# Kernel tuning notes

Measured on AMD Instinct MI355X. Metric: run time of the kernel, lower is better.

Reference implementation:

```python
import jax, jax.numpy as jnp
import numpy as np

PAD = 1
THRESH = 10.0


def setup_inputs() -> dict:
    key = jax.random.key(0)
    k1, k2, k3 = jax.random.split(key, 3)
    x = jax.random.normal(k1, (8, 16, 62, 62), dtype=jnp.float32)
    W = jax.random.normal(k2, (32, 16, 3, 3), dtype=jnp.float32)
    b = jax.random.normal(k3, (32,), dtype=jnp.float32)
    return {"x": x, "W": W, "b": b}


def reference(x, W, b):
    # ZeroPad2d(padding) on all four sides
    x = jnp.pad(x, ((0, 0), (0, 0), (PAD, PAD), (PAD, PAD)))
    T, C, xr, xc = x.shape
    O, _, wr, wc = W.shape
    L = xr * xc

    # get_xfft_thresh: 1D FFT over flattened HxW, zero coeffs with |Re| < thresh
    xf = jnp.fft.fft(x.reshape(T, C, L))                      # (T,C,L) complex
    xf = jnp.where(jnp.abs(xf.real) < THRESH, jnp.zeros_like(xf), xf)

    # get_Wfft: zero-pad kernel to (xr,xc) bottom/right, flatten, reverse along
    # length (flipud(flip([0,1])) nets to a flip of the last axis only), then FFT
    Wp = jnp.pad(W, ((0, 0), (0, 0), (0, xr - wr), (0, xc - wc))).reshape(O, C, L)
    Wf = jnp.fft.fft(Wp[:, :, ::-1])                          # (O,C,L) complex

    # fftConv1D, batched over (image, out_channel):
    y = jnp.fft.ifft(xf[:, None, :, :] * Wf[None, :, :, :]).real  # (T,O,C,L)
    # torch.roll(y, 1) with no dims rolls the FLATTENED (C*L) tensor by 1
    y = jnp.roll(y.reshape(T, O, C * L), 1, axis=-1).reshape(T, O, C, xr, xc)
    y = y.sum(axis=2)                                         # sum over in-channels
    ans_r, ans_c = xr - wr + 1, xc - wc + 1
    y = y[:, :, :ans_r, :ans_c]
    return y + b[None, :, None, None]
```

## Files before the change

kernel.cpp:

```cpp
#include <hip/hip_runtime.h>
#include <math.h>

#define TWO_PI 6.28318530717958647692f
#define NT     512
#define WPB    8
#define RPW    8
#define PITCH  65
#define THRESH 10.0f

__device__ __forceinline__ int brev6(int x) {
    return (int)(__brev((unsigned)x) >> 26);
}

__device__ __forceinline__ void cfma(float& dr, float& di, float ar, float ai,
                                     float br, float bi) {
    dr = fmaf(ar, br, fmaf(-ai, bi, dr));
    di = fmaf(ar, bi, fmaf(ai, br, di));
}

__device__ __forceinline__ void fft64_dif(float (&re)[RPW], float (&im)[RPW],
                                          int lane, float sign) {
    #pragma unroll
    for (int h = 32; h >= 1; h >>= 1) {
        int j = lane & (h - 1);
        float ang = sign * (TWO_PI / 64.0f) * (float)(j * (32 / h));
        float wr, wi;
        __sincosf(ang, &wi, &wr);
        bool upper = (lane & h) != 0;
        float cwr = upper ? wr : 1.0f;
        float cwi = upper ? wi : 0.0f;
        float sgn = upper ? -1.0f : 1.0f;
        #pragma unroll
        for (int m = 0; m < RPW; ++m) {
            float orr = __shfl_xor(re[m], h, 64);
            float oii = __shfl_xor(im[m], h, 64);
            float ar = fmaf(sgn, re[m], orr);
            float ai = fmaf(sgn, im[m], oii);
            re[m] = ar * cwr - ai * cwi;
            im[m] = ar * cwi + ai * cwr;
        }
    }
}

__device__ __forceinline__ void fft64_dit(float (&re)[RPW], float (&im)[RPW],
                                          int lane, float sign) {
    #pragma unroll
    for (int h = 1; h <= 32; h <<= 1) {
        int j = lane & (h - 1);
        float ang = sign * (TWO_PI / 64.0f) * (float)(j * (32 / h));
        float wr, wi;
        __sincosf(ang, &wi, &wr);
        bool upper = (lane & h) != 0;
        float cwr = upper ? wr : 1.0f;
        float cwi = upper ? wi : 0.0f;
        float sgn = upper ? -1.0f : 1.0f;
        #pragma unroll
        for (int m = 0; m < RPW; ++m) {
            float tr = re[m] * cwr - im[m] * cwi;
            float ti = re[m] * cwi + im[m] * cwr;
            float orr = __shfl_xor(tr, h, 64);
            float oii = __shfl_xor(ti, h, 64);
            re[m] = fmaf(sgn, tr, orr);
            im[m] = fmaf(sgn, ti, oii);
        }
    }
}

__global__ __launch_bounds__(NT) void fwd_kernel(const float* __restrict__ x,
                                                 float2* __restrict__ X) {
    __shared__ float sre[64 * PITCH];
    __shared__ float sim[64 * PITCH];
    const int tc   = blockIdx.x;
    const int tid  = threadIdx.x;
    const int lane = tid & 63;
    const int w    = tid >> 6;
    const float* xrow = x + (size_t)tc * 62 * 62;

    for (int idx = tid; idx < 4096; idx += NT) {
        int r = idx >> 6, s = idx & 63;
        float v = 0.0f;
        if (r >= 1 && r <= 62 && s >= 1 && s <= 62)
            v = xrow[(r - 1) * 62 + (s - 1)];
        sre[r * PITCH + s] = v;
    }
    __syncthreads();

    float re[RPW], im[RPW];
    #pragma unroll
    for (int m = 0; m < RPW; ++m) {
        re[m] = sre[lane * PITCH + (w * RPW + m)];
        im[m] = 0.0f;
    }
    fft64_dif(re, im, lane, -1.0f);
    const int k1 = brev6(lane);
    #pragma unroll
    for (int m = 0; m < RPW; ++m) {
        int n2 = w * RPW + m;
        float cr, ci;
        __sincosf(-(TWO_PI / 4096.0f) * (float)(k1 * n2), &ci, &cr);
        float rr = re[m] * cr - im[m] * ci;
        im[m]    = re[m] * ci + im[m] * cr;
        re[m]    = rr;
    }
    __syncthreads();
    #pragma unroll
    for (int m = 0; m < RPW; ++m) {
        int n2 = w * RPW + m;
        sre[k1 * PITCH + n2] = re[m];
        sim[k1 * PITCH + n2] = im[m];
    }
    __syncthreads();
    #pragma unroll
    for (int m = 0; m < RPW; ++m) {
        int row = w * RPW + m;
        re[m] = sre[row * PITCH + lane];
        im[m] = sim[row * PITCH + lane];
    }
    fft64_dif(re, im, lane, -1.0f);
    float2* Xrow = X + (size_t)tc * 4096;
    #pragma unroll
    for (int m = 0; m < RPW; ++m) {
        int row = w * RPW + m;
        float rr = re[m], ii = im[m];
        if (fabsf(rr) < THRESH) { rr = 0.0f; ii = 0.0f; }
        Xrow[row * 64 + lane] = make_float2(rr, ii);
    }
}

__global__ __launch_bounds__(NT) void conv_kernel(const float2* __restrict__ X,
                                                  const float* __restrict__ W,
                                                  const float* __restrict__ b,
                                                  float* __restrict__ out) {
    __shared__ float sre[64 * PITCH];
    __shared__ float sim[64 * PITCH];
    __shared__ float Wsh[144];
    const int t    = blockIdx.x >> 5;
    const int o    = blockIdx.x & 31;
    const int tid  = threadIdx.x;
    const int lane = tid & 63;
    const int w    = tid >> 6;
    if (tid < 144) Wsh[tid] = W[o * 144 + tid];
    __syncthreads();

    const int k2 = brev6(lane);
    float elr, eli;
    __sincosf((TWO_PI / 64.0f) * (float)k2, &eli, &elr);

    float re[RPW], im[RPW];
    const float2* Xt = X + (size_t)t * 16 * 4096;
    #pragma unroll
    for (int m = 0; m < RPW; ++m) {
        const int k1 = w * RPW + m;
        float ur, ui, vkr, vki;
        __sincosf((TWO_PI / 64.0f) * (float)k1, &ui, &ur);
        __sincosf((TWO_PI / 4096.0f) * (float)k1, &vki, &vkr);
        float vr = vkr * elr - vki * eli;
        float vi = vkr * eli + vki * elr;
        float qr[9] = {0,0,0,0,0,0,0,0,0};
        float qi[9] = {0,0,0,0,0,0,0,0,0};
        const int p = k1 * 64 + lane;
        #pragma unroll
        for (int c = 0; c < 16; ++c) {
            float2 xc = Xt[c * 4096 + p];
            const float* wc = &Wsh[c * 9];
            #pragma unroll
            for (int q = 0; q < 9; ++q) {
                qr[q] = fmaf(wc[q], xc.x, qr[q]);
                qi[q] = fmaf(wc[q], xc.y, qi[q]);
            }
        }
        float R0r, R0i, R1r, R1i, R2r, R2i, tr_, ti_;
        tr_ = qr[2]; ti_ = qi[2];
        R0r = qr[1]; R0i = qi[1]; cfma(R0r, R0i, vr, vi, tr_, ti_);
        tr_ = R0r; ti_ = R0i;
        R0r = qr[0]; R0i = qi[0]; cfma(R0r, R0i, vr, vi, tr_, ti_);
        tr_ = qr[5]; ti_ = qi[5];
        R1r = qr[4]; R1i = qi[4]; cfma(R1r, R1i, vr, vi, tr_, ti_);
        tr_ = R1r; ti_ = R1i;
        R1r = qr[3]; R1i = qi[3]; cfma(R1r, R1i, vr, vi, tr_, ti_);
        tr_ = qr[8]; ti_ = qi[8];
        R2r = qr[7]; R2i = qi[7]; cfma(R2r, R2i, vr, vi, tr_, ti_);
        tr_ = R2r; ti_ = R2i;
        R2r = qr[6]; R2i = qi[6]; cfma(R2r, R2i, vr, vi, tr_, ti_);
        cfma(R1r, R1i, ur, ui, R2r, R2i);
        cfma(R0r, R0i, ur, ui, R1r, R1i);
        re[m] = R0r;
        im[m] = R0i;
    }
    fft64_dit(re, im, lane, +1.0f);
    #pragma unroll
    for (int m = 0; m < RPW; ++m) {
        int k1 = w * RPW + m;
        float cr, ci;
        __sincosf((TWO_PI / 4096.0f) * (float)(k1 * lane), &ci, &cr);
        float rr = re[m] * cr - im[m] * ci;
        im[m]    = re[m] * ci + im[m] * cr;
        re[m]    = rr;
    }
    #pragma unroll
    for (int m = 0; m < RPW; ++m) {
        int k1 = w * RPW + m;
        sre[k1 * PITCH + lane] = re[m];
        sim[k1 * PITCH + lane] = im[m];
    }
    __syncthreads();
    #pragma unroll
    for (int m = 0; m < RPW; ++m) {
        int n2 = w * RPW + m;
        re[m] = sre[lane * PITCH + n2];
        im[m] = sim[lane * PITCH + n2];
    }
    fft64_dif(re, im, lane, +1.0f);
    __syncthreads();
    const int n1 = brev6(lane);
    #pragma unroll
    for (int m = 0; m < RPW; ++m) {
        int n2 = w * RPW + m;
        sre[n1 * PITCH + n2] = re[m];
    }
    __syncthreads();
    const float bias = b[o];
    float* orow = out + (size_t)blockIdx.x * 62 * 62;
    for (int idx = tid; idx < 62 * 62; idx += NT) {
        int r = idx / 62, s = idx - r * 62;
        orow[idx] = sre[r * PITCH + s] * (1.0f / 4096.0f) + bias;
    }
}

extern "C" void kernel_launch(void* const* d_in, const int* in_sizes, int n_in,
                              void* d_out, int out_size, void* d_ws, size_t ws_size,
                              hipStream_t stream) {
    const float* x = (const float*)d_in[0];
    const float* W = (const float*)d_in[1];
    const float* b = (const float*)d_in[2];
    float* out = (float*)d_out;
    float2* X = (float2*)d_ws;

    fwd_kernel<<<dim3(128), dim3(NT), 0, stream>>>(x, X);
    conv_kernel<<<dim3(256), dim3(NT), 0, stream>>>(X, W, b, out);
}
```

Baseline: 87.60 us.

## Restructure conv accumulation per channel and replace per-element sincos with recurrences

```diff
diff --git a/kernel.cpp b/kernel.cpp
--- a/kernel.cpp
+++ b/kernel.cpp
@@ -3,19 +3,16 @@
 
 #define TWO_PI 6.28318530717958647692f
 #define NT     512
-#define WPB    8
 #define RPW    8
 #define PITCH  65
 #define THRESH 10.0f
+#define C64    0.995184726672196886f
+#define S64    0.098017140329560602f
+#define C4096  0.999998823451701879f
+#define S4096  0.001533980186284766f
 
 __device__ __forceinline__ int brev6(int x) {
     return (int)(__brev((unsigned)x) >> 26);
-}
-
-__device__ __forceinline__ void cfma(float& dr, float& di, float ar, float ai,
-                                     float br, float bi) {
-    dr = fmaf(ar, br, fmaf(-ai, bi, dr));
-    di = fmaf(ar, bi, fmaf(ai, br, di));
 }
 
 __device__ __forceinline__ void fft64_dif(float (&re)[RPW], float (&im)[RPW],
@@ -93,14 +90,18 @@
     }
     fft64_dif(re, im, lane, -1.0f);
     const int k1 = brev6(lane);
-    #pragma unroll
-    for (int m = 0; m < RPW; ++m) {
-        int n2 = w * RPW + m;
-        float cr, ci;
-        __sincosf(-(TWO_PI / 4096.0f) * (float)(k1 * n2), &ci, &cr);
-        float rr = re[m] * cr - im[m] * ci;
-        im[m]    = re[m] * ci + im[m] * cr;
-        re[m]    = rr;
+    {
+        float cr, ci, sr, si;
+        __sincosf(-(TWO_PI / 512.0f) * (float)(k1 * w), &ci, &cr);
+        __sincosf(-(TWO_PI / 4096.0f) * (float)k1, &si, &sr);
+        #pragma unroll
+        for (int m = 0; m < RPW; ++m) {
+            float rr = re[m] * cr - im[m] * ci;
+            im[m]    = re[m] * ci + im[m] * cr;
+            re[m]    = rr;
+            float nr = cr * sr - ci * si;
+            ci = cr * si + ci * sr; cr = nr;
+        }
     }
     __syncthreads();
     #pragma unroll
@@ -127,75 +128,94 @@
     }
 }
 
-__global__ __launch_bounds__(NT) void conv_kernel(const float2* __restrict__ X,
-                                                  const float* __restrict__ W,
-                                                  const float* __restrict__ b,
-                                                  float* __restrict__ out) {
+__global__ __launch_bounds__(NT, 4) void conv_kernel(const float2* __restrict__ X,
+                                                     const float* __restrict__ W,
+                                                     const float* __restrict__ b,
+                                                     float* __restrict__ out) {
     __shared__ float sre[64 * PITCH];
     __shared__ float sim[64 * PITCH];
-    __shared__ float Wsh[144];
+    __shared__ __align__(16) float Wsh[16 * 12];
     const int t    = blockIdx.x >> 5;
     const int o    = blockIdx.x & 31;
     const int tid  = threadIdx.x;
     const int lane = tid & 63;
     const int w    = tid >> 6;
-    if (tid < 144) Wsh[tid] = W[o * 144 + tid];
+    if (tid < 144) {
+        int c = tid / 9, q = tid - c * 9;
+        Wsh[c * 12 + q] = W[o * 144 + tid];
+    }
     __syncthreads();
 
     const int k2 = brev6(lane);
     float elr, eli;
     __sincosf((TWO_PI / 64.0f) * (float)k2, &eli, &elr);
 
+    float ur[RPW], ui[RPW], vr[RPW], vi[RPW], v2r[RPW], v2i[RPW];
+    {
+        float cur, cui, cvr, cvi;
+        __sincosf((TWO_PI / 8.0f) * (float)w, &cui, &cur);
+        __sincosf((TWO_PI / 512.0f) * (float)w, &cvi, &cvr);
+        #pragma unroll
+        for (int m = 0; m < RPW; ++m) {
+            ur[m] = cur; ui[m] = cui;
+            float vvr = cvr * elr - cvi * eli;
+            float vvi = cvr * eli + cvi * elr;
+            vr[m] = vvr; vi[m] = vvi;
+            v2r[m] = vvr * vvr - vvi * vvi;
+            v2i[m] = 2.0f * vvr * vvi;
+            float nur = cur * C64 - cui * S64;
+            cui = cur * S64 + cui * C64; cur = nur;
+            float nvr = cvr * C4096 - cvi * S4096;
+            cvi = cvr * S4096 + cvi * C4096; cvr = nvr;
+        }
+    }
+
+    float Sr[RPW], Si[RPW];
+    #pragma unroll
+    for (int m = 0; m < RPW; ++m) { Sr[m] = 0.0f; Si[m] = 0.0f; }
+
+    const float2* Xt = X + (size_t)t * 16 * 4096 + (w * (RPW * 64) + lane);
+    #pragma unroll 1
+    for (int c = 0; c < 16; ++c) {
+        const float4* wp = (const float4*)&Wsh[c * 12];
+        float4 wa = wp[0];
+        float4 wb = wp[1];
+        float  w8 = wp[2].x;
+        const float2* xp = Xt + c * 4096;
+        #pragma unroll
+        for (int m = 0; m < RPW; ++m) {
+            float2 xv = xp[m * 64];
+            float h0r = fmaf(v2r[m], wa.z, fmaf(vr[m], wa.y, wa.x));
+            float h0i = fmaf(v2i[m], wa.z, vi[m] * wa.y);
+            float h1r = fmaf(v2r[m], wb.y, fmaf(vr[m], wb.x, wa.w));
+            float h1i = fmaf(v2i[m], wb.y, vi[m] * wb.x);
+            float h2r = fmaf(v2r[m], w8, fmaf(vr[m], wb.w, wb.z));
+            float h2i = fmaf(v2i[m], w8, vi[m] * wb.w);
+            float inr = fmaf(ur[m], h2r, fmaf(-ui[m], h2i, h1r));
+            float ini = fmaf(ur[m], h2i, fmaf( ui[m], h2r, h1i));
+            float Pr  = fmaf(ur[m], inr, fmaf(-ui[m], ini, h0r));
+            float Pi  = fmaf(ur[m], ini, fmaf( ui[m], inr, h0i));
+            Sr[m] = fmaf(xv.x, Pr, fmaf(-xv.y, Pi, Sr[m]));
+            Si[m] = fmaf(xv.x, Pi, fmaf( xv.y, Pr, Si[m]));
+        }
+    }
+
     float re[RPW], im[RPW];
-    const float2* Xt = X + (size_t)t * 16 * 4096;
-    #pragma unroll
-    for (int m = 0; m < RPW; ++m) {
-        const int k1 = w * RPW + m;
-        float ur, ui, vkr, vki;
-        __sincosf((TWO_PI / 64.0f) * (float)k1, &ui, &ur);
-        __sincosf((TWO_PI / 4096.0f) * (float)k1, &vki, &vkr);
-        float vr = vkr * elr - vki * eli;
-        float vi = vkr * eli + vki * elr;
-        float qr[9] = {0,0,0,0,0,0,0,0,0};
-        float qi[9] = {0,0,0,0,0,0,0,0,0};
-        const int p = k1 * 64 + lane;
-        #pragma unroll
-        for (int c = 0; c < 16; ++c) {
-            float2 xc = Xt[c * 4096 + p];
-            const float* wc = &Wsh[c * 9];
-            #pragma unroll
-            for (int q = 0; q < 9; ++q) {
-                qr[q] = fmaf(wc[q], xc.x, qr[q]);
-                qi[q] = fmaf(wc[q], xc.y, qi[q]);
-            }
-        }
-        float R0r, R0i, R1r, R1i, R2r, R2i, tr_, ti_;
-        tr_ = qr[2]; ti_ = qi[2];
-        R0r = qr[1]; R0i = qi[1]; cfma(R0r, R0i, vr, vi, tr_, ti_);
-        tr_ = R0r; ti_ = R0i;
-        R0r = qr[0]; R0i = qi[0]; cfma(R0r, R0i, vr, vi, tr_, ti_);
-        tr_ = qr[5]; ti_ = qi[5];
-        R1r = qr[4]; R1i = qi[4]; cfma(R1r, R1i, vr, vi, tr_, ti_);
-        tr_ = R1r; ti_ = R1i;
-        R1r = qr[3]; R1i = qi[3]; cfma(R1r, R1i, vr, vi, tr_, ti_);
-        tr_ = qr[8]; ti_ = qi[8];
-        R2r = qr[7]; R2i = qi[7]; cfma(R2r, R2i, vr, vi, tr_, ti_);
-        tr_ = R2r; ti_ = R2i;
-        R2r = qr[6]; R2i = qi[6]; cfma(R2r, R2i, vr, vi, tr_, ti_);
-        cfma(R1r, R1i, ur, ui, R2r, R2i);
-        cfma(R0r, R0i, ur, ui, R1r, R1i);
-        re[m] = R0r;
-        im[m] = R0i;
-    }
+    #pragma unroll
+    for (int m = 0; m < RPW; ++m) { re[m] = Sr[m]; im[m] = Si[m]; }
     fft64_dit(re, im, lane, +1.0f);
-    #pragma unroll
-    for (int m = 0; m < RPW; ++m) {
-        int k1 = w * RPW + m;
-        float cr, ci;
-        __sincosf((TWO_PI / 4096.0f) * (float)(k1 * lane), &ci, &cr);
-        float rr = re[m] * cr - im[m] * ci;
-        im[m]    = re[m] * ci + im[m] * cr;
-        re[m]    = rr;
+    {
+        float cr, ci, sr, si;
+        __sincosf((TWO_PI / 512.0f) * (float)(lane * w), &ci, &cr);
+        __sincosf((TWO_PI / 4096.0f) * (float)lane, &si, &sr);
+        #pragma unroll
+        for (int m = 0; m < RPW; ++m) {
+            float rr = re[m] * cr - im[m] * ci;
+            im[m]    = re[m] * ci + im[m] * cr;
+            re[m]    = rr;
+            float nr = cr * sr - ci * si;
+            ci = cr * si + ci * sr; cr = nr;
+        }
     }
     #pragma unroll
     for (int m = 0; m < RPW; ++m) {
```

Result: slower. 91.15 us (+4.0%).

## Use 1024-thread blocks with packed float2 math and streamed channel loads

Applied to the files above, without the earlier changes.

```diff
diff --git a/kernel.cpp b/kernel.cpp
--- a/kernel.cpp
+++ b/kernel.cpp
@@ -2,23 +2,27 @@
 #include <math.h>
 
 #define TWO_PI 6.28318530717958647692f
-#define NT     512
-#define WPB    8
-#define RPW    8
+#define NT     1024
+#define RPW    4
 #define PITCH  65
 #define THRESH 10.0f
+#define C4096  0.999998823451701879f
+#define S4096  0.001533980186284766f
+
+typedef float v2f __attribute__((ext_vector_type(2)));
 
 __device__ __forceinline__ int brev6(int x) {
     return (int)(__brev((unsigned)x) >> 26);
 }
 
-__device__ __forceinline__ void cfma(float& dr, float& di, float ar, float ai,
-                                     float br, float bi) {
-    dr = fmaf(ar, br, fmaf(-ai, bi, dr));
-    di = fmaf(ar, bi, fmaf(ai, br, di));
-}
-
-__device__ __forceinline__ void fft64_dif(float (&re)[RPW], float (&im)[RPW],
+__device__ __forceinline__ v2f cmul_add(v2f a, v2f b, v2f acc) {
+    acc += (v2f){a.x, a.x} * b;
+    acc += (v2f){a.y, a.y} * (v2f){-b.y, b.x};
+    return acc;
+}
+
+template<int R>
+__device__ __forceinline__ void fft64_dif(float (&re)[R], float (&im)[R],
                                           int lane, float sign) {
     #pragma unroll
     for (int h = 32; h >= 1; h >>= 1) {
@@ -31,7 +35,7 @@
         float cwi = upper ? wi : 0.0f;
         float sgn = upper ? -1.0f : 1.0f;
         #pragma unroll
-        for (int m = 0; m < RPW; ++m) {
+        for (int m = 0; m < R; ++m) {
             float orr = __shfl_xor(re[m], h, 64);
             float oii = __shfl_xor(im[m], h, 64);
             float ar = fmaf(sgn, re[m], orr);
@@ -42,7 +46,8 @@
     }
 }
 
-__device__ __forceinline__ void fft64_dit(float (&re)[RPW], float (&im)[RPW],
+template<int R>
+__device__ __forceinline__ void fft64_dit(float (&re)[R], float (&im)[R],
                                           int lane, float sign) {
     #pragma unroll
     for (int h = 1; h <= 32; h <<= 1) {
@@ -55,7 +60,7 @@
         float cwi = upper ? wi : 0.0f;
         float sgn = upper ? -1.0f : 1.0f;
         #pragma unroll
-        for (int m = 0; m < RPW; ++m) {
+        for (int m = 0; m < R; ++m) {
             float tr = re[m] * cwr - im[m] * cwi;
             float ti = re[m] * cwi + im[m] * cwr;
             float orr = __shfl_xor(tr, h, 64);
@@ -70,17 +75,17 @@
                                                  float2* __restrict__ X) {
     __shared__ float sre[64 * PITCH];
     __shared__ float sim[64 * PITCH];
-    const int tc   = blockIdx.x;
+    const int task = blockIdx.x;
     const int tid  = threadIdx.x;
     const int lane = tid & 63;
     const int w    = tid >> 6;
-    const float* xrow = x + (size_t)tc * 62 * 62;
+    const float* xr = x + (size_t)task * 62 * 62;
 
     for (int idx = tid; idx < 4096; idx += NT) {
         int r = idx >> 6, s = idx & 63;
         float v = 0.0f;
         if (r >= 1 && r <= 62 && s >= 1 && s <= 62)
-            v = xrow[(r - 1) * 62 + (s - 1)];
+            v = xr[(r - 1) * 62 + (s - 1)];
         sre[r * PITCH + s] = v;
     }
     __syncthreads();
@@ -91,7 +96,7 @@
         re[m] = sre[lane * PITCH + (w * RPW + m)];
         im[m] = 0.0f;
     }
-    fft64_dif(re, im, lane, -1.0f);
+    fft64_dif<RPW>(re, im, lane, -1.0f);
     const int k1 = brev6(lane);
     #pragma unroll
     for (int m = 0; m < RPW; ++m) {
@@ -116,8 +121,8 @@
         re[m] = sre[row * PITCH + lane];
         im[m] = sim[row * PITCH + lane];
     }
-    fft64_dif(re, im, lane, -1.0f);
-    float2* Xrow = X + (size_t)tc * 4096;
+    fft64_dif<RPW>(re, im, lane, -1.0f);
+    float2* Xrow = X + (size_t)task * 4096;
     #pragma unroll
     for (int m = 0; m < RPW; ++m) {
         int row = w * RPW + m;
@@ -127,75 +132,71 @@
     }
 }
 
-__global__ __launch_bounds__(NT) void conv_kernel(const float2* __restrict__ X,
-                                                  const float* __restrict__ W,
-                                                  const float* __restrict__ b,
-                                                  float* __restrict__ out) {
+__global__ __launch_bounds__(NT, 4) void conv_kernel(const float2* __restrict__ X,
+                                                     const float* __restrict__ W,
+                                                     const float* __restrict__ b,
+                                                     float* __restrict__ out) {
     __shared__ float sre[64 * PITCH];
     __shared__ float sim[64 * PITCH];
-    __shared__ float Wsh[144];
     const int t    = blockIdx.x >> 5;
     const int o    = blockIdx.x & 31;
     const int tid  = threadIdx.x;
     const int lane = tid & 63;
     const int w    = tid >> 6;
-    if (tid < 144) Wsh[tid] = W[o * 144 + tid];
-    __syncthreads();
 
     const int k2 = brev6(lane);
     float elr, eli;
     __sincosf((TWO_PI / 64.0f) * (float)k2, &eli, &elr);
 
+    const float2* Xt = X + (size_t)t * 16 * 4096 + lane;
+    const float*  wo = W + o * 144;
+
     float re[RPW], im[RPW];
-    const float2* Xt = X + (size_t)t * 16 * 4096;
     #pragma unroll
     for (int m = 0; m < RPW; ++m) {
         const int k1 = w * RPW + m;
+        v2f Q0 = {0,0}, Q1 = {0,0}, Q2 = {0,0}, Q3 = {0,0}, Q4 = {0,0};
+        v2f Q5 = {0,0}, Q6 = {0,0}, Q7 = {0,0}, Q8 = {0,0};
+        const float2* xp = Xt + k1 * 64;
+        v2f xb;
+        { float2 q = xp[0]; xb = (v2f){q.x, q.y}; }
+        #pragma unroll 1
+        for (int c = 0; c < 16; ++c) {
+            v2f xn;
+            if (c < 15) { float2 q = xp[(c + 1) * 4096]; xn = (v2f){q.x, q.y}; }
+            const float* wc = wo + c * 9;
+            Q0 += xb * wc[0]; Q1 += xb * wc[1]; Q2 += xb * wc[2];
+            Q3 += xb * wc[3]; Q4 += xb * wc[4]; Q5 += xb * wc[5];
+            Q6 += xb * wc[6]; Q7 += xb * wc[7]; Q8 += xb * wc[8];
+            xb = xn;
+        }
         float ur, ui, vkr, vki;
         __sincosf((TWO_PI / 64.0f) * (float)k1, &ui, &ur);
         __sincosf((TWO_PI / 4096.0f) * (float)k1, &vki, &vkr);
-        float vr = vkr * elr - vki * eli;
-        float vi = vkr * eli + vki * elr;
-        float qr[9] = {0,0,0,0,0,0,0,0,0};
-        float qi[9] = {0,0,0,0,0,0,0,0,0};
-        const int p = k1 * 64 + lane;
+        v2f u  = {ur, ui};
+        v2f v  = {vkr * elr - vki * eli, vkr * eli + vki * elr};
+        v2f v2 = {v.x * v.x - v.y * v.y, 2.0f * v.x * v.y};
+        v2f h0 = cmul_add(v2, Q2, cmul_add(v, Q1, Q0));
+        v2f h1 = cmul_add(v2, Q5, cmul_add(v, Q4, Q3));
+        v2f h2 = cmul_add(v2, Q8, cmul_add(v, Q7, Q6));
+        v2f S  = cmul_add(u, cmul_add(u, h2, h1), h0);
+        re[m] = S.x;
+        im[m] = S.y;
+    }
+
+    fft64_dit<RPW>(re, im, lane, +1.0f);
+    {
+        float cr, ci, sr, si;
+        __sincosf((TWO_PI / 1024.0f) * (float)(lane * w), &ci, &cr);
+        __sincosf((TWO_PI / 4096.0f) * (float)lane, &si, &sr);
         #pragma unroll
-        for (int c = 0; c < 16; ++c) {
-            float2 xc = Xt[c * 4096 + p];
-            const float* wc = &Wsh[c * 9];
-            #pragma unroll
-            for (int q = 0; q < 9; ++q) {
-                qr[q] = fmaf(wc[q], xc.x, qr[q]);
-                qi[q] = fmaf(wc[q], xc.y, qi[q]);
-            }
-        }
-        float R0r, R0i, R1r, R1i, R2r, R2i, tr_, ti_;
-        tr_ = qr[2]; ti_ = qi[2];
-        R0r = qr[1]; R0i = qi[1]; cfma(R0r, R0i, vr, vi, tr_, ti_);
-        tr_ = R0r; ti_ = R0i;
-        R0r = qr[0]; R0i = qi[0]; cfma(R0r, R0i, vr, vi, tr_, ti_);
-        tr_ = qr[5]; ti_ = qi[5];
-        R1r = qr[4]; R1i = qi[4]; cfma(R1r, R1i, vr, vi, tr_, ti_);
-        tr_ = R1r; ti_ = R1i;
-        R1r = qr[3]; R1i = qi[3]; cfma(R1r, R1i, vr, vi, tr_, ti_);
-        tr_ = qr[8]; ti_ = qi[8];
-        R2r = qr[7]; R2i = qi[7]; cfma(R2r, R2i, vr, vi, tr_, ti_);
-        tr_ = R2r; ti_ = R2i;
-        R2r = qr[6]; R2i = qi[6]; cfma(R2r, R2i, vr, vi, tr_, ti_);
-        cfma(R1r, R1i, ur, ui, R2r, R2i);
-        cfma(R0r, R0i, ur, ui, R1r, R1i);
-        re[m] = R0r;
-        im[m] = R0i;
-    }
-    fft64_dit(re, im, lane, +1.0f);
-    #pragma unroll
-    for (int m = 0; m < RPW; ++m) {
-        int k1 = w * RPW + m;
-        float cr, ci;
-        __sincosf((TWO_PI / 4096.0f) * (float)(k1 * lane), &ci, &cr);
-        float rr = re[m] * cr - im[m] * ci;
-        im[m]    = re[m] * ci + im[m] * cr;
-        re[m]    = rr;
+        for (int m = 0; m < RPW; ++m) {
+            float rr = re[m] * cr - im[m] * ci;
+            im[m]    = re[m] * ci + im[m] * cr;
+            re[m]    = rr;
+            float nr = cr * sr - ci * si;
+            ci = cr * si + ci * sr; cr = nr;
+        }
     }
     #pragma unroll
     for (int m = 0; m < RPW; ++m) {
@@ -210,7 +211,7 @@
         re[m] = sre[lane * PITCH + n2];
         im[m] = sim[lane * PITCH + n2];
     }
-    fft64_dif(re, im, lane, +1.0f);
+    fft64_dif<RPW>(re, im, lane, +1.0f);
     __syncthreads();
     const int n1 = brev6(lane);
     #pragma unroll
```

Result: slower. 96.18 us (+9.8%).
